# Kernel optimization log

Hardware: AMD Instinct MI355X
Metric: run time of the kernel (lower is better)

## Reference

```python
import jax, jax.numpy as jnp
import numpy as np

CI_SCALE = 1.0


def _rot_y(a):
    c, s = np.cos(a), np.sin(a)
    return np.array([[c, 0.0, s], [0.0, 1.0, 0.0], [-s, 0.0, c]], dtype=np.float32)


def setup_inputs() -> dict:
    key = jax.random.key(0)
    B, V, C, Hs, Ws = 1, 3, 32, 256, 256
    Ht, Wt, D = 128, 128, 48
    src_feat = jax.random.normal(key, (B, V, C, Hs, Ws), dtype=jnp.float32)
    # Realistic pinhole cameras so the plane-sweep warp lands in-frame.
    Ks = np.array([[200.0, 0.0, Ws / 2], [0.0, 200.0, Hs / 2], [0.0, 0.0, 1.0]], dtype=np.float32)
    Kt = np.array([[100.0, 0.0, Wt / 2], [0.0, 100.0, Ht / 2], [0.0, 0.0, 1.0]], dtype=np.float32)
    src_exts = np.zeros((B, V, 4, 4), dtype=np.float32)
    for i in range(V):
        R = _rot_y(0.1 * (i - (V - 1) / 2))
        src_exts[0, i, :3, :3] = R
        src_exts[0, i, :3, 3] = np.array([-0.3 * (i - (V - 1) / 2), 0.0, 0.0], dtype=np.float32)
        src_exts[0, i, 3, 3] = 1.0
    tar_exts = np.eye(4, dtype=np.float32)[None]
    return {
        "src_feat": src_feat,
        "src_exts": jnp.asarray(src_exts),
        "src_ints": jnp.asarray(np.broadcast_to(Ks, (B, V, 3, 3)).copy()),
        "tar_exts": jnp.asarray(tar_exts),
        "tar_ints": jnp.asarray(Kt[None].copy()),
        "near_far": jnp.broadcast_to(jnp.array([2.0, 6.0], dtype=jnp.float32).reshape(1, 2, 1, 1), (B, 2, Ht, Wt)),
        "num_depth": D,
    }


def _grid_sample_zeros(feat, grid):
    """Bilinear, padding_mode='zeros', align_corners=False.
    feat: (N,C,Hs,Ws); grid: (N,Hg,Wg,2) normalized -> (N,C,Hg,Wg)."""
    N, C, Hs, Ws = feat.shape
    gx = jnp.clip((grid[..., 0] + 1.0) * (Ws / 2) - 0.5, -1e6, 1e6)
    gy = jnp.clip((grid[..., 1] + 1.0) * (Hs / 2) - 0.5, -1e6, 1e6)
    x0f, y0f = jnp.floor(gx), jnp.floor(gy)
    wx, wy = gx - x0f, gy - y0f
    x0, y0 = x0f.astype(jnp.int32), y0f.astype(jnp.int32)
    x1, y1 = x0 + 1, y0 + 1
    b = jnp.arange(N)[:, None, None]

    def tap(yi, xi):
        valid = (xi >= 0) & (xi < Ws) & (yi >= 0) & (yi < Hs)
        v = feat[b, :, jnp.clip(yi, 0, Hs - 1), jnp.clip(xi, 0, Ws - 1)]  # (N,Hg,Wg,C)
        return v * valid[..., None]

    out = (tap(y0, x0) * ((1 - wy) * (1 - wx))[..., None]
           + tap(y0, x1) * ((1 - wy) * wx)[..., None]
           + tap(y1, x0) * (wy * (1 - wx))[..., None]
           + tap(y1, x1) * (wy * wx)[..., None])
    return jnp.transpose(out, (0, 3, 1, 2))


def _build_feature_volume(src_feat, src_exts, src_ints, tar_exts, tar_ints, depth_values):
    B, V, C, Hs, Ws = src_feat.shape
    D, Ht, Wt = depth_values.shape[1:]
    src_projs = src_ints @ src_exts[..., :3, :]                       # (B,V,3,4)
    tar34 = tar_ints @ tar_exts[:, :3, :]                             # (B,3,4)
    bottom = jnp.broadcast_to(jnp.array([0.0, 0.0, 0.0, 1.0], dtype=tar34.dtype).reshape(1, 1, 4), (B, 1, 4))
    tar_proj = jnp.concatenate([tar34, bottom], axis=1)               # (B,4,4)
    proj = (src_projs @ jnp.linalg.inv(tar_proj)[:, None]).reshape(B * V, 3, 4)
    xs = jnp.arange(Wt, dtype=src_feat.dtype) + 0.5
    ys = jnp.arange(Ht, dtype=src_feat.dtype) + 0.5
    gx, gy = jnp.meshgrid(xs, ys, indexing='xy')                      # (Ht,Wt)
    xyz = jnp.stack([gx, gy, jnp.ones_like(gx)], 0).reshape(3, Ht * Wt)
    dvals = jnp.broadcast_to(depth_values.reshape(B, 1, D, Ht * Wt), (B, V, D, Ht * Wt)).reshape(B * V, 1, D, Ht * Wt)
    p = proj[:, :, :3] @ xyz                                          # (BV,3,HW)
    p = p[:, :, None, :] * dvals + proj[:, :, 3:, None]               # (BV,3,D,HW)
    p = jnp.transpose(p, (0, 2, 3, 1))                                # (BV,D,HW,3)
    z = jnp.maximum(p[..., 2:3], 1e-6)
    g = p[..., :2] / z
    grid = jnp.stack([2 * g[..., 0] / Ws - 1, 2 * g[..., 1] / Hs - 1], -1)  # (BV,D,HW,2)
    warped = _grid_sample_zeros(src_feat.reshape(B * V, C, Hs, Ws), grid)   # (BV,C,D,HW)
    warped = warped.reshape(B, V, C, D, Ht, Wt)
    return jnp.var(warped, axis=1)                                    # (B,C,D,Ht,Wt), unbiased=False


def reference(src_feat, src_exts, src_ints, tar_exts, tar_ints, near_far, num_depth):
    B, _, Ht, Wt = near_far.shape
    t = jnp.linspace(0.0, 1.0, num_depth, dtype=near_far.dtype).reshape(1, num_depth, 1, 1)
    depth_values = near_far[:, :1] + (near_far[:, -1:] - near_far[:, :1]) * t   # (B,D,Ht,Wt)
    vol = _build_feature_volume(src_feat, src_exts, src_ints, tar_exts, tar_ints, depth_values)
    prob = jax.nn.softmax(-vol.mean(axis=1), axis=1)                  # (B,D,Ht,Wt)
    depth = jnp.sum(prob * depth_values, axis=1, keepdims=True)       # (B,1,Ht,Wt)
    var = jnp.sum(prob * jnp.square(depth_values - depth), axis=1, keepdims=True)
    half_ci = CI_SCALE * jnp.sqrt(jnp.maximum(var, 1e-12))
    ci = jnp.concatenate([jnp.maximum(depth - half_ci, depth_values[:, :1]),
                          jnp.minimum(depth + half_ci, depth_values[:, -1:])], axis=1)
    return depth, ci
```

## Files before the change

### kernel.cpp

```cpp
#include <hip/hip_runtime.h>
#include <math.h>

#define NV 3
#define NC 32
#define HS 256
#define WS 256
#define HT 128
#define WT 128
#define ND 48
#define NPIX (HT*WT)
#define HSP 259
#define WSP 259
#define ROW4 (WSP*8)
#define IMG4 (HSP*ROW4)
#define FEAT_T_ELEMS (NV*IMG4*4)
#define NB_INTERIOR 6144
#define NBORDER_PIX (3*(3*WSP + 3*HS))
#define NBORDER_F4  (NBORDER_PIX*8)
#define NB_BORDER   145

__global__ __launch_bounds__(256) void prep(
        const float* __restrict__ src, float* __restrict__ dstf,
        const float* __restrict__ src_exts,
        const float* __restrict__ src_ints,
        const float* __restrict__ tar_exts,
        const float* __restrict__ tar_ints,
        float* __restrict__ proj_out) {
    float4* dst = (float4*)dstf;
    int bid = blockIdx.x;
    if (bid < NB_INTERIOR) {
        int g = bid*256 + threadIdx.x;
        int q = g & 7;
        int x = (g >> 3) & (WS-1);
        int y = (g >> 11) & (HS-1);
        int v = g >> 19;
        const float* sp = src + (((size_t)(v*NC + q*4))*HS + y)*WS + x;
        float a = sp[0];
        float b = sp[HS*WS];
        float c = sp[2*HS*WS];
        float d = sp[3*HS*WS];
        dst[(v*HSP + y+1)*WSP*8 + (x+1)*8 + q] = make_float4(a,b,c,d);
        return;
    }
    int t = (bid - NB_INTERIOR)*256 + threadIdx.x;
    if (t < NBORDER_F4) {
        int pixb = t >> 3, q = t & 7;
        int v = pixb / (NBORDER_PIX/3);
        int r = pixb - v*(NBORDER_PIX/3);
        int y, x;
        if (r < 3*WSP) {
            int band = r / WSP;
            y = (band == 0) ? 0 : (band == 1 ? 257 : 258);
            x = r - band*WSP;
        } else {
            int rr = r - 3*WSP;
            int band = rr >> 8;
            x = (band == 0) ? 0 : (band == 1 ? 257 : 258);
            y = 1 + (rr & 255);
        }
        dst[(v*HSP + y)*WSP*8 + x*8 + q] = make_float4(0.f,0.f,0.f,0.f);
    }
    if (bid == NB_INTERIOR && threadIdx.x == 0) {
        float Kt[9], Et[16];
        for (int i = 0; i < 9;  i++) Kt[i] = tar_ints[i];
        for (int i = 0; i < 16; i++) Et[i] = tar_exts[i];
        float T[12];
        for (int rI = 0; rI < 3; rI++)
            for (int col = 0; col < 4; col++) {
                float s = 0.f;
                for (int k = 0; k < 3; k++) s += Kt[rI*3+k] * Et[k*4+col];
                T[rI*4+col] = s;
            }
        float M[9]  = {T[0],T[1],T[2], T[4],T[5],T[6], T[8],T[9],T[10]};
        float tv[3] = {T[3],T[7],T[11]};
        float det = M[0]*(M[4]*M[8]-M[5]*M[7])
                  - M[1]*(M[3]*M[8]-M[5]*M[6])
                  + M[2]*(M[3]*M[7]-M[4]*M[6]);
        float id = 1.0f/det;
        float Mi[9];
        Mi[0] =  (M[4]*M[8]-M[5]*M[7])*id;
        Mi[1] = -(M[1]*M[8]-M[2]*M[7])*id;
        Mi[2] =  (M[1]*M[5]-M[2]*M[4])*id;
        Mi[3] = -(M[3]*M[8]-M[5]*M[6])*id;
        Mi[4] =  (M[0]*M[8]-M[2]*M[6])*id;
        Mi[5] = -(M[0]*M[5]-M[2]*M[3])*id;
        Mi[6] =  (M[3]*M[7]-M[4]*M[6])*id;
        Mi[7] = -(M[0]*M[7]-M[1]*M[6])*id;
        Mi[8] =  (M[0]*M[4]-M[1]*M[3])*id;
        float mt[3];
        for (int rI = 0; rI < 3; rI++)
            mt[rI] = -(Mi[rI*3+0]*tv[0] + Mi[rI*3+1]*tv[1] + Mi[rI*3+2]*tv[2]);
        float inv4[16] = {Mi[0],Mi[1],Mi[2],mt[0],
                          Mi[3],Mi[4],Mi[5],mt[1],
                          Mi[6],Mi[7],Mi[8],mt[2],
                          0.f,0.f,0.f,1.f};
        for (int v = 0; v < NV; v++) {
            const float* Ks = src_ints + v*9;
            const float* Ev = src_exts + v*16;
            float P34[12];
            for (int rI = 0; rI < 3; rI++)
                for (int col = 0; col < 4; col++) {
                    float s = 0.f;
                    for (int k = 0; k < 3; k++) s += Ks[rI*3+k] * Ev[k*4+col];
                    P34[rI*4+col] = s;
                }
            for (int rI = 0; rI < 3; rI++)
                for (int col = 0; col < 4; col++) {
                    float s = 0.f;
                    for (int k = 0; k < 4; k++) s += P34[rI*4+k] * inv4[k*4+col];
                    proj_out[v*12 + rI*4 + col] = s;
                }
        }
    }
}

__global__ __launch_bounds__(256, 6) void depth_main(
        const float4* __restrict__ featT,
        const float* __restrict__ proj,
        const float* __restrict__ near_far,
        float* __restrict__ out) {
    __shared__ float cl[8][56];

    const int tid  = threadIdx.x;
    const int w    = tid >> 6;
    const int lane = tid & 63;
    const int p    = lane >> 3;
    const int q    = lane & 7;

    const int pix = blockIdx.x*8 + p;
    const float cx = (pix & (WT-1)) + 0.5f;
    const float cy = (pix >> 7) + 0.5f;

    float rx[NV], ry[NV], rz[NV], tx[NV], ty[NV], tz[NV];
    #pragma unroll
    for (int v = 0; v < NV; v++) {
        const float* P = proj + v*12;
        rx[v] = P[0]*cx + P[1]*cy + P[2];  tx[v] = P[3];
        ry[v] = P[4]*cx + P[5]*cy + P[6];  ty[v] = P[7];
        rz[v] = P[8]*cx + P[9]*cy + P[10]; tz[v] = P[11];
    }

    const float nearv = near_far[pix];
    const float farv  = near_far[NPIX + pix];
    const float step  = (farv - nearv) * (1.0f/(ND-1));
    const float d0    = (float)(w*12);

    #pragma unroll 2
    for (int dd = 0; dd < 12; dd++) {
        const float dv = fmaf(step, d0 + (float)dd, nearv);
        float ax=0.f, ay=0.f, az=0.f, aw=0.f;
        float mxs=0.f, mys=0.f, mzs=0.f, mws=0.f;
        #pragma unroll
        for (int v = 0; v < NV; v++) {
            float pxx = fmaf(rx[v], dv, tx[v]);
            float pyy = fmaf(ry[v], dv, ty[v]);
            float pzz = fmaf(rz[v], dv, tz[v]);
            float z    = fmaxf(pzz, 1e-6f);
            float invz = 1.0f / z;
            float sx = fminf(fmaxf(fmaf(pxx, invz, -0.5f), -1.0f), 256.0f);
            float sy = fminf(fmaxf(fmaf(pyy, invz, -0.5f), -1.0f), 256.0f);
            float x0f = floorf(sx), y0f = floorf(sy);
            float wx = sx - x0f,   wy = sy - y0f;
            int xi = (int)x0f + 1;
            int yi = (int)y0f + 1;
            int r0 = v*IMG4 + yi*ROW4 + xi*8 + q;
            int r1 = r0 + ROW4;
            float4 f00 = featT[r0];
            float4 f01 = featT[r0 + 8];
            float4 f10 = featT[r1];
            float4 f11 = featT[r1 + 8];
            float w11 = wx*wy;
            float w10 = wy - w11;
            float w01 = wx - w11;
            float w00 = (1.0f - wx) - w10;
            float vx = f00.x*w00 + f01.x*w01 + f10.x*w10 + f11.x*w11;
            float vy = f00.y*w00 + f01.y*w01 + f10.y*w10 + f11.y*w11;
            float vz = f00.z*w00 + f01.z*w01 + f10.z*w10 + f11.z*w11;
            float vw = f00.w*w00 + f01.w*w01 + f10.w*w10 + f11.w*w11;
            ax = fmaf(vx,vx,ax); ay = fmaf(vy,vy,ay);
            az = fmaf(vz,vz,az); aw = fmaf(vw,vw,aw);
            mxs += vx; mys += vy; mzs += vz; mws += vw;
        }
        float a  = (ax + ay) + (az + aw);
        float m2 = mxs*mxs + mys*mys + mzs*mzs + mws*mws;
        #pragma unroll
        for (int s = 1; s < 8; s <<= 1) {
            a  += __shfl_xor(a,  s, 64);
            m2 += __shfl_xor(m2, s, 64);
        }
        float cost = (a*(1.0f/3.0f) - m2*(1.0f/9.0f)) * (1.0f/32.0f);
        if (q == 0) cl[p][w*12 + dd] = cost;
    }

    __syncthreads();
    if (w != 0) return;

    float n[6], dvs[6];
    #pragma unroll
    for (int j = 0; j < 6; j++) {
        n[j]   = -cl[p][q + 8*j];
        dvs[j] = fmaf(step, (float)(q + 8*j), nearv);
    }
    float mx = n[0];
    #pragma unroll
    for (int j = 1; j < 6; j++) mx = fmaxf(mx, n[j]);
    #pragma unroll
    for (int s = 1; s < 8; s <<= 1) mx = fmaxf(mx, __shfl_xor(mx, s, 64));
    float e[6];
    float s0 = 0.f, s1 = 0.f;
    #pragma unroll
    for (int j = 0; j < 6; j++) {
        e[j] = __expf(n[j] - mx);
        s0 += e[j];
        s1 = fmaf(e[j], dvs[j], s1);
    }
    #pragma unroll
    for (int s = 1; s < 8; s <<= 1) {
        s0 += __shfl_xor(s0, s, 64);
        s1 += __shfl_xor(s1, s, 64);
    }
    float depth = s1 / s0;
    float s2 = 0.f;
    #pragma unroll
    for (int j = 0; j < 6; j++) {
        float qd = dvs[j] - depth;
        s2 = fmaf(e[j]*qd, qd, s2);
    }
    #pragma unroll
    for (int s = 1; s < 8; s <<= 1) s2 += __shfl_xor(s2, s, 64);
    float var = s2 / s0;
    float hci = sqrtf(fmaxf(var, 1e-12f));
    if (q == 0) {
        out[pix]          = depth;
        out[NPIX + pix]   = fmaxf(depth - hci, nearv);
        out[2*NPIX + pix] = fminf(depth + hci, farv);
    }
}

extern "C" void kernel_launch(void* const* d_in, const int* in_sizes, int n_in,
                              void* d_out, int out_size, void* d_ws, size_t ws_size,
                              hipStream_t stream) {
    const float* src_feat = (const float*)d_in[0];
    const float* src_exts = (const float*)d_in[1];
    const float* src_ints = (const float*)d_in[2];
    const float* tar_exts = (const float*)d_in[3];
    const float* tar_ints = (const float*)d_in[4];
    const float* near_far = (const float*)d_in[5];
    float* out   = (float*)d_out;
    float* featT = (float*)d_ws;
    float* proj  = featT + FEAT_T_ELEMS;

    hipLaunchKernelGGL(prep, dim3(NB_INTERIOR + NB_BORDER), dim3(256), 0, stream,
                       src_feat, featT, src_exts, src_ints, tar_exts, tar_ints, proj);
    hipLaunchKernelGGL(depth_main, dim3(NPIX/8), dim3(256), 0, stream,
                       (const float4*)featT, proj, near_far, out);
}
```

Before: 130.9 us.

## Swizzle depth blocks per XCD, coalesce prep writes, use DPP reductions

The depth kernel's block index is remapped so blocks landing on the same XCD under round-robin dispatch cover contiguous pixel rows. This is meant to improve L2 reuse of the gathered feature taps. The prep kernel now has each block transpose one source row with strided loops, for more regular loads and stores. The 8-lane shuffle reductions in both the cost and softmax stages are replaced with DPP quad_perm/row_half_mirror ops to avoid LDS-backed permutes, and the per-lane q offset is folded into the base pointer.

Measured after the change: 123.9 us. -5.3%, faster.

```diff
diff --git a/kernel.cpp b/kernel.cpp
--- a/kernel.cpp
+++ b/kernel.cpp
@@ -14,10 +14,31 @@
 #define ROW4 (WSP*8)
 #define IMG4 (HSP*ROW4)
 #define FEAT_T_ELEMS (NV*IMG4*4)
-#define NB_INTERIOR 6144
+#define NB_INTERIOR (NV*HS)
 #define NBORDER_PIX (3*(3*WSP + 3*HS))
 #define NBORDER_F4  (NBORDER_PIX*8)
 #define NB_BORDER   145
+
+__device__ __forceinline__ float dpp_sum8(float x) {
+    int v;
+    v = __builtin_amdgcn_update_dpp(0, __float_as_int(x), 0xB1,  0xF, 0xF, true);
+    x += __int_as_float(v);
+    v = __builtin_amdgcn_update_dpp(0, __float_as_int(x), 0x4E,  0xF, 0xF, true);
+    x += __int_as_float(v);
+    v = __builtin_amdgcn_update_dpp(0, __float_as_int(x), 0x141, 0xF, 0xF, true);
+    x += __int_as_float(v);
+    return x;
+}
+__device__ __forceinline__ float dpp_max8(float x) {
+    int v;
+    v = __builtin_amdgcn_update_dpp(0, __float_as_int(x), 0xB1,  0xF, 0xF, true);
+    x = fmaxf(x, __int_as_float(v));
+    v = __builtin_amdgcn_update_dpp(0, __float_as_int(x), 0x4E,  0xF, 0xF, true);
+    x = fmaxf(x, __int_as_float(v));
+    v = __builtin_amdgcn_update_dpp(0, __float_as_int(x), 0x141, 0xF, 0xF, true);
+    x = fmaxf(x, __int_as_float(v));
+    return x;
+}
 
 __global__ __launch_bounds__(256) void prep(
         const float* __restrict__ src, float* __restrict__ dstf,
@@ -29,17 +50,21 @@
     float4* dst = (float4*)dstf;
     int bid = blockIdx.x;
     if (bid < NB_INTERIOR) {
-        int g = bid*256 + threadIdx.x;
-        int q = g & 7;
-        int x = (g >> 3) & (WS-1);
-        int y = (g >> 11) & (HS-1);
-        int v = g >> 19;
-        const float* sp = src + (((size_t)(v*NC + q*4))*HS + y)*WS + x;
-        float a = sp[0];
-        float b = sp[HS*WS];
-        float c = sp[2*HS*WS];
-        float d = sp[3*HS*WS];
-        dst[(v*HSP + y+1)*WSP*8 + (x+1)*8 + q] = make_float4(a,b,c,d);
+        int v  = bid >> 8;
+        int y  = bid & 255;
+        int x0 = threadIdx.x & 31;
+        int q  = threadIdx.x >> 5;
+        const float* in = src + ((size_t)(v*NC + q*4))*HS*WS + (size_t)y*WS;
+        float4* drow = dst + (size_t)(v*HSP + y+1)*ROW4 + 8 + q;
+        #pragma unroll
+        for (int it = 0; it < 8; it++) {
+            int x = it*32 + x0;
+            float a = in[x];
+            float b = in[HS*WS   + x];
+            float c = in[2*HS*WS + x];
+            float d = in[3*HS*WS + x];
+            drow[x*8] = make_float4(a,b,c,d);
+        }
         return;
     }
     int t = (bid - NB_INTERIOR)*256 + threadIdx.x;
@@ -127,7 +152,8 @@
     const int p    = lane >> 3;
     const int q    = lane & 7;
 
-    const int pix = blockIdx.x*8 + p;
+    const int lb  = ((blockIdx.x & 7) << 8) | (blockIdx.x >> 3);
+    const int pix = lb*8 + p;
     const float cx = (pix & (WT-1)) + 0.5f;
     const float cy = (pix >> 7) + 0.5f;
 
@@ -144,6 +170,8 @@
     const float farv  = near_far[NPIX + pix];
     const float step  = (farv - nearv) * (1.0f/(ND-1));
     const float d0    = (float)(w*12);
+
+    const float4* base0 = featT + q;
 
     #pragma unroll 2
     for (int dd = 0; dd < 12; dd++) {
@@ -163,12 +191,12 @@
             float wx = sx - x0f,   wy = sy - y0f;
             int xi = (int)x0f + 1;
             int yi = (int)y0f + 1;
-            int r0 = v*IMG4 + yi*ROW4 + xi*8 + q;
+            int r0 = v*IMG4 + yi*ROW4 + xi*8;
             int r1 = r0 + ROW4;
-            float4 f00 = featT[r0];
-            float4 f01 = featT[r0 + 8];
-            float4 f10 = featT[r1];
-            float4 f11 = featT[r1 + 8];
+            float4 f00 = base0[r0];
+            float4 f01 = base0[r0 + 8];
+            float4 f10 = base0[r1];
+            float4 f11 = base0[r1 + 8];
             float w11 = wx*wy;
             float w10 = wy - w11;
             float w01 = wx - w11;
@@ -181,13 +209,8 @@
             az = fmaf(vz,vz,az); aw = fmaf(vw,vw,aw);
             mxs += vx; mys += vy; mzs += vz; mws += vw;
         }
-        float a  = (ax + ay) + (az + aw);
-        float m2 = mxs*mxs + mys*mys + mzs*mzs + mws*mws;
-        #pragma unroll
-        for (int s = 1; s < 8; s <<= 1) {
-            a  += __shfl_xor(a,  s, 64);
-            m2 += __shfl_xor(m2, s, 64);
-        }
+        float a  = dpp_sum8((ax + ay) + (az + aw));
+        float m2 = dpp_sum8(mxs*mxs + mys*mys + mzs*mzs + mws*mws);
         float cost = (a*(1.0f/3.0f) - m2*(1.0f/9.0f)) * (1.0f/32.0f);
         if (q == 0) cl[p][w*12 + dd] = cost;
     }
@@ -204,8 +227,7 @@
     float mx = n[0];
     #pragma unroll
     for (int j = 1; j < 6; j++) mx = fmaxf(mx, n[j]);
-    #pragma unroll
-    for (int s = 1; s < 8; s <<= 1) mx = fmaxf(mx, __shfl_xor(mx, s, 64));
+    mx = dpp_max8(mx);
     float e[6];
     float s0 = 0.f, s1 = 0.f;
     #pragma unroll
@@ -214,11 +236,8 @@
         s0 += e[j];
         s1 = fmaf(e[j], dvs[j], s1);
     }
-    #pragma unroll
-    for (int s = 1; s < 8; s <<= 1) {
-        s0 += __shfl_xor(s0, s, 64);
-        s1 += __shfl_xor(s1, s, 64);
-    }
+    s0 = dpp_sum8(s0);
+    s1 = dpp_sum8(s1);
     float depth = s1 / s0;
     float s2 = 0.f;
     #pragma unroll
@@ -226,8 +245,7 @@
         float qd = dvs[j] - depth;
         s2 = fmaf(e[j]*qd, qd, s2);
     }
-    #pragma unroll
-    for (int s = 1; s < 8; s <<= 1) s2 += __shfl_xor(s2, s, 64);
+    s2 = dpp_sum8(s2);
     float var = s2 / s0;
     float hci = sqrtf(fmaxf(var, 1e-12f));
     if (q == 0) {
```
